# Optimization experiments

Measured on AMD Instinct MI355X. Metric: run time of the kernel, lower is better.

## Reference

```python
import jax, jax.numpy as jnp
import numpy as np

N_EMBD = 16
NQ = 4  # n_qubits
# Qiskit 'circular' entangler map for 4 qubits, 2-qubit blocks
PAIRS = [(3, 0), (0, 1), (1, 2), (2, 3)]
PI = float(np.pi)
_par = np.array([1.0, -1.0], np.float32)
PARITY = np.einsum('a,b,c,d->abcd', _par, _par, _par, _par)  # Z^x4 eigenvalues


def _apply_1q(state, U, q):
    # state: (2,2,2,2) complex; apply 2x2 U on qubit axis q
    return jnp.moveaxis(jnp.tensordot(U, state, axes=[[1], [q]]), 0, q)


def _apply_p(state, lam, q):
    # phase gate diag(1, e^{i lam}) on qubit q
    e = jnp.exp(1j * lam)
    fac = jnp.stack([jnp.ones((), e.dtype), e])
    fac = fac.reshape([2 if a == q else 1 for a in range(NQ)])
    return state * fac


def _apply_cx(state, c, t):
    s0 = jax.lax.index_in_dim(state, 0, axis=c, keepdims=True)
    s1 = jnp.flip(jax.lax.index_in_dim(state, 1, axis=c, keepdims=True), axis=t)
    return jnp.concatenate([s0, s1], axis=c)


def _ry(th):
    c = jnp.cos(th / 2)
    s = jnp.sin(th / 2)
    return jnp.stack([jnp.stack([c, -s]), jnp.stack([s, c])]).astype(jnp.complex64)


def _qnn_expval(x4, w):
    # exact 4-qubit statevector sim of ZZFeatureMap(reps=1, circular) +
    # RealAmplitudes(reps=2, circular); observable Z^{x4}
    state = jnp.zeros((2,) * NQ, jnp.complex64).at[0, 0, 0, 0].set(1.0)
    Hm = jnp.asarray(np.array([[1, 1], [1, -1]], np.complex64) / np.sqrt(2, dtype=np.float32))
    for q in range(NQ):
        state = _apply_1q(state, Hm, q)
    for q in range(NQ):
        state = _apply_p(state, 2.0 * x4[q], q)
    for (i, j) in PAIRS:
        state = _apply_cx(state, i, j)
        state = _apply_p(state, 2.0 * (PI - x4[i]) * (PI - x4[j]), j)
        state = _apply_cx(state, i, j)
    for rep in range(2):
        for q in range(NQ):
            state = _apply_1q(state, _ry(w[4 * rep + q]), q)
        for (i, j) in PAIRS:
            state = _apply_cx(state, i, j)
    for q in range(NQ):
        state = _apply_1q(state, _ry(w[8 + q]), q)
    probs = state.real ** 2 + state.imag ** 2
    return jnp.sum(jnp.asarray(PARITY) * probs)


def setup_inputs() -> dict:
    key = jax.random.key(0)
    k0, k1, k2, k3, k4 = jax.random.split(key, 5)
    B, T, C, H = 65536, 8, N_EMBD, 16
    scale = 1.0 / np.sqrt(C)
    return {
        'x': jax.random.normal(k0, (B, T, C), jnp.float32),
        'Wk': jax.random.normal(k1, (C, H), jnp.float32) * scale,
        'Wq': jax.random.normal(k2, (C, H), jnp.float32) * scale,
        'Wv': jax.random.normal(k3, (C, H), jnp.float32) * scale,
        'qnn_w': 0.1 * jax.random.normal(k4, (12,), jnp.float32),
        'quantum_scale': jnp.asarray(0.1, jnp.float32),
    }


def reference(x, Wk, Wq, Wv, qnn_w, quantum_scale):
    B, T, C = x.shape
    k = x @ Wk  # [B,T,H]
    q = x @ Wq
    v = x @ Wv
    scores = jnp.einsum('bth,bsh->bts', q, k) * (C ** -0.5)
    mask = jnp.tril(jnp.ones((T, T), bool))
    scores = jnp.where(mask, scores, -jnp.inf)
    wei = jax.nn.softmax(scores, axis=-1)
    # quantum enhancement: per-batch features = tanh(mean_h q)[:, :4]
    qf = jnp.tanh(jnp.mean(q, axis=-1)[:, :NQ])  # [B, 4]
    ev = jax.vmap(lambda f: _qnn_expval(f, qnn_w))(qf)  # [B]
    # original appends identical output min(T,4) times per b -> mean over b
    enh = jax.nn.sigmoid(jnp.mean(ev)) * quantum_scale
    wei = wei + enh  # dropout: eval mode (identity)
    return jnp.einsum('bts,bsh->bth', wei, v)
```

## Files before the change

### kernel.cpp

```cpp
#include <hip/hip_runtime.h>
#include <math.h>

#define T 8
#define C 16
#define H 16

__global__ __launch_bounds__(256) void qnn_kernel(
    const float* __restrict__ x,
    const float* __restrict__ Wq,
    const float* __restrict__ qw,
    float* __restrict__ evsum,
    int B)
{
  __shared__ float wqm[16];
  __shared__ float wsum[4];
  int tid = threadIdx.x;
  if (tid < 16) {
    float s = 0.f;
    #pragma unroll
    for (int h = 0; h < 16; ++h) s += Wq[tid*16 + h];
    wqm[tid] = s * (1.0f/16.0f);
  }
  __syncthreads();

  int b = blockIdx.x * 256 + tid;
  float ev = 0.f;
  if (b < B) {
    const float* xb = x + (size_t)b * (T*C);
    float f[4];
    #pragma unroll
    for (int j = 0; j < 4; ++j) {
      float d = 0.f;
      #pragma unroll
      for (int c4 = 0; c4 < 4; ++c4) {
        float4 xv = ((const float4*)(xb + j*16))[c4];
        d += xv.x*wqm[c4*4+0] + xv.y*wqm[c4*4+1] + xv.z*wqm[c4*4+2] + xv.w*wqm[c4*4+3];
      }
      f[j] = tanhf(d);
    }
    const float PI_F = 3.14159265358979323846f;
    float l30 = 2.f*(PI_F - f[3])*(PI_F - f[0]);
    float l01 = 2.f*(PI_F - f[0])*(PI_F - f[1]);
    float l12 = 2.f*(PI_F - f[1])*(PI_F - f[2]);
    float l23 = 2.f*(PI_F - f[2])*(PI_F - f[3]);
    float sr[16], si[16];
    #pragma unroll
    for (int z = 0; z < 16; ++z) {
      int b0 = (z>>3)&1, b1 = (z>>2)&1, b2 = (z>>1)&1, b3 = z&1;
      float ph = 2.f*(f[0]*b0 + f[1]*b1 + f[2]*b2 + f[3]*b3)
               + l30*(float)(b3^b0) + l01*(float)(b0^b1)
               + l12*(float)(b1^b2) + l23*(float)(b2^b3);
      float cp, sp;
      __sincosf(ph, &sp, &cp);
      sr[z] = 0.25f * cp;
      si[z] = 0.25f * sp;
    }
    #pragma unroll
    for (int rep = 0; rep < 3; ++rep) {
      #pragma unroll
      for (int q = 0; q < 4; ++q) {
        float th = 0.5f * qw[rep*4 + q];
        float cth = cosf(th), sth = sinf(th);
        int m = 8 >> q;
        #pragma unroll
        for (int z = 0; z < 16; ++z) {
          if (z & m) continue;
          int z1 = z | m;
          float a0r = sr[z],  a0i = si[z];
          float a1r = sr[z1], a1i = si[z1];
          sr[z]  = cth*a0r - sth*a1r;  si[z]  = cth*a0i - sth*a1i;
          sr[z1] = sth*a0r + cth*a1r;  si[z1] = sth*a0i + cth*a1i;
        }
      }
      if (rep < 2) {
        #pragma unroll
        for (int p = 0; p < 4; ++p) {
          const int ctl[4] = {3,0,1,2};
          const int tgt[4] = {0,1,2,3};
          int mc = 8 >> ctl[p], mt = 8 >> tgt[p];
          #pragma unroll
          for (int z = 0; z < 16; ++z) {
            if ((z & mc) && !(z & mt)) {
              int z1 = z | mt;
              float tr = sr[z]; sr[z] = sr[z1]; sr[z1] = tr;
              float ti = si[z]; si[z] = si[z1]; si[z1] = ti;
            }
          }
        }
      }
    }
    #pragma unroll
    for (int z = 0; z < 16; ++z) {
      float p = sr[z]*sr[z] + si[z]*si[z];
      ev += (__popc(z) & 1) ? -p : p;
    }
  }
  #pragma unroll
  for (int off = 32; off > 0; off >>= 1) ev += __shfl_down(ev, off, 64);
  if ((tid & 63) == 0) wsum[tid >> 6] = ev;
  __syncthreads();
  if (tid == 0) atomicAdd(evsum, wsum[0] + wsum[1] + wsum[2] + wsum[3]);
}

#define GB 32
__global__ __launch_bounds__(256) void attn_kernel(
    const float* __restrict__ x,
    const float* __restrict__ Wk,
    const float* __restrict__ Wq,
    const float* __restrict__ Wv,
    const float* __restrict__ evsum,
    const float* __restrict__ qscale,
    float* __restrict__ out,
    float invB)
{
  __shared__ float ks[GB][132];
  __shared__ float vs[GB][132];
  int tid = threadIdx.x;
  int g = tid >> 3, t = tid & 7;
  size_t b = (size_t)blockIdx.x * GB + g;
  const float* xp = x + (b*T + t) * C;

  float xr[16];
  #pragma unroll
  for (int i = 0; i < 4; ++i) {
    float4 v4 = ((const float4*)xp)[i];
    xr[4*i+0] = v4.x; xr[4*i+1] = v4.y; xr[4*i+2] = v4.z; xr[4*i+3] = v4.w;
  }

  float kr[16], qr[16], vr[16];
  #pragma unroll
  for (int h = 0; h < 16; ++h) { kr[h] = 0.f; qr[h] = 0.f; vr[h] = 0.f; }
  #pragma unroll
  for (int c = 0; c < 16; ++c) {
    float xc = xr[c];
    #pragma unroll
    for (int h = 0; h < 16; ++h) {
      kr[h] += xc * Wk[c*16 + h];
      qr[h] += xc * Wq[c*16 + h];
      vr[h] += xc * Wv[c*16 + h];
    }
  }
  #pragma unroll
  for (int i = 0; i < 4; ++i) {
    ((float4*)&ks[g][t*16])[i] = make_float4(kr[4*i], kr[4*i+1], kr[4*i+2], kr[4*i+3]);
    ((float4*)&vs[g][t*16])[i] = make_float4(vr[4*i], vr[4*i+1], vr[4*i+2], vr[4*i+3]);
  }
  __syncthreads();

  float enh = qscale[0] / (1.f + __expf(-evsum[0] * invB));

  float sc[8];
  #pragma unroll
  for (int s = 0; s < 8; ++s) {
    float d = 0.f;
    #pragma unroll
    for (int i = 0; i < 4; ++i) {
      float4 kv = ((const float4*)&ks[g][s*16])[i];
      d += qr[4*i]*kv.x + qr[4*i+1]*kv.y + qr[4*i+2]*kv.z + qr[4*i+3]*kv.w;
    }
    sc[s] = d * 0.25f;
  }
  float m = sc[0];
  #pragma unroll
  for (int s = 1; s < 8; ++s) if (s <= t) m = fmaxf(m, sc[s]);
  float w8[8], sum = 0.f;
  #pragma unroll
  for (int s = 0; s < 8; ++s) {
    float e = (s <= t) ? __expf(sc[s] - m) : 0.f;
    w8[s] = e; sum += e;
  }
  float inv = 1.f / sum;
  #pragma unroll
  for (int s = 0; s < 8; ++s) w8[s] = w8[s]*inv + enh;

  float acc[16];
  #pragma unroll
  for (int h = 0; h < 16; ++h) acc[h] = 0.f;
  #pragma unroll
  for (int s = 0; s < 8; ++s) {
    float w = w8[s];
    #pragma unroll
    for (int i = 0; i < 4; ++i) {
      float4 vv = ((const float4*)&vs[g][s*16])[i];
      acc[4*i+0] += w*vv.x; acc[4*i+1] += w*vv.y;
      acc[4*i+2] += w*vv.z; acc[4*i+3] += w*vv.w;
    }
  }
  float* op = out + (b*T + t) * C;
  #pragma unroll
  for (int i = 0; i < 4; ++i)
    ((float4*)op)[i] = make_float4(acc[4*i], acc[4*i+1], acc[4*i+2], acc[4*i+3]);
}

extern "C" void kernel_launch(void* const* d_in, const int* in_sizes, int n_in,
                              void* d_out, int out_size, void* d_ws, size_t ws_size,
                              hipStream_t stream) {
  const float* x  = (const float*)d_in[0];
  const float* Wk = (const float*)d_in[1];
  const float* Wq = (const float*)d_in[2];
  const float* Wv = (const float*)d_in[3];
  const float* qw = (const float*)d_in[4];
  const float* qs = (const float*)d_in[5];
  float* out = (float*)d_out;
  float* evsum = (float*)d_ws;

  int B = in_sizes[0] / (T * C);

  hipMemsetAsync(evsum, 0, sizeof(float), stream);
  qnn_kernel<<<(B + 255) / 256, 256, 0, stream>>>(x, Wq, qw, evsum, B);
  attn_kernel<<<B / GB, 256, 0, stream>>>(x, Wk, Wq, Wv, evsum, qs, out,
                                          1.0f / (float)B);
}
```

Baseline: 121.8 us.

## Rewrite attention kernel with bf16 MFMA tiles and fused Wq·Wkᵀ

```diff
diff --git a/kernel.cpp b/kernel.cpp
--- a/kernel.cpp
+++ b/kernel.cpp
@@ -1,16 +1,26 @@
 #include <hip/hip_runtime.h>
+#include <hip/hip_bf16.h>
 #include <math.h>
 
 #define T 8
 #define C 16
-#define H 16
+
+typedef __attribute__((ext_vector_type(4))) float f32x4;
+typedef __attribute__((ext_vector_type(8))) short s16x8;
+
+__device__ inline unsigned int pkbf(float a, float b) {
+  __hip_bfloat162 h = __float22bfloat162_rn(make_float2(a, b));
+  unsigned int u; __builtin_memcpy(&u, &h, 4); return u;
+}
+__device__ inline s16x8 mk_frag(float a0, float a1, float a2, float a3) {
+  union { s16x8 v; unsigned int u[4]; } f;
+  f.u[0] = pkbf(a0, a1); f.u[1] = pkbf(a2, a3); f.u[2] = 0u; f.u[3] = 0u;
+  return f.v;
+}
 
 __global__ __launch_bounds__(256) void qnn_kernel(
-    const float* __restrict__ x,
-    const float* __restrict__ Wq,
-    const float* __restrict__ qw,
-    float* __restrict__ evsum,
-    int B)
+    const float* __restrict__ x, const float* __restrict__ Wq,
+    const float* __restrict__ qw, float* __restrict__ evsum, int B)
 {
   __shared__ float wqm[16];
   __shared__ float wsum[4];
@@ -36,7 +46,8 @@
         float4 xv = ((const float4*)(xb + j*16))[c4];
         d += xv.x*wqm[c4*4+0] + xv.y*wqm[c4*4+1] + xv.z*wqm[c4*4+2] + xv.w*wqm[c4*4+3];
       }
-      f[j] = tanhf(d);
+      float e2 = __expf(2.f*d);
+      f[j] = 1.f - 2.f/(e2 + 1.f);
     }
     const float PI_F = 3.14159265358979323846f;
     float l30 = 2.f*(PI_F - f[3])*(PI_F - f[0]);
@@ -52,8 +63,7 @@
                + l12*(float)(b1^b2) + l23*(float)(b2^b3);
       float cp, sp;
       __sincosf(ph, &sp, &cp);
-      sr[z] = 0.25f * cp;
-      si[z] = 0.25f * sp;
+      sr[z] = 0.25f * cp; si[z] = 0.25f * sp;
     }
     #pragma unroll
     for (int rep = 0; rep < 3; ++rep) {
@@ -102,94 +112,83 @@
   if (tid == 0) atomicAdd(evsum, wsum[0] + wsum[1] + wsum[2] + wsum[3]);
 }
 
-#define GB 32
-__global__ __launch_bounds__(256) void attn_kernel(
+#define TPW 4
+__global__ __launch_bounds__(256) void attn_mfma(
     const float* __restrict__ x,
-    const float* __restrict__ Wk,
-    const float* __restrict__ Wq,
+    const float* __restrict__ Wk, const float* __restrict__ Wq,
     const float* __restrict__ Wv,
-    const float* __restrict__ evsum,
-    const float* __restrict__ qscale,
-    float* __restrict__ out,
-    float invB)
+    const float* __restrict__ evsum, const float* __restrict__ qscale,
+    float* __restrict__ out, float invB, int ntiles)
 {
-  __shared__ float ks[GB][132];
-  __shared__ float vs[GB][132];
-  int tid = threadIdx.x;
-  int g = tid >> 3, t = tid & 7;
-  size_t b = (size_t)blockIdx.x * GB + g;
-  const float* xp = x + (b*T + t) * C;
-
-  float xr[16];
+  const int lane = threadIdx.x & 63;
+  const int wid  = threadIdx.x >> 6;
+  const int r16  = lane & 15;
+  const int g    = lane >> 4;
+
+  const float enh = qscale[0] / (1.f + __expf(-evsum[0] * invB));
+
+  const float4 wq4 = *(const float4*)(Wq + r16*16 + 4*g);
+  const float4 wk4 = *(const float4*)(Wk + r16*16 + 4*g);
+  s16x8 aWq = mk_frag(wq4.x, wq4.y, wq4.z, wq4.w);
+  s16x8 bWk = mk_frag(wk4.x, wk4.y, wk4.z, wk4.w);
+  f32x4 zero = {0.f, 0.f, 0.f, 0.f};
+  f32x4 M = __builtin_amdgcn_mfma_f32_16x16x32_bf16(aWq, bWk, zero, 0, 0, 0);
+  s16x8 aMt = mk_frag(0.25f*M[0], 0.25f*M[1], 0.25f*M[2], 0.25f*M[3]);
+  const float wv0 = Wv[(4*g+0)*16 + r16];
+  const float wv1 = Wv[(4*g+1)*16 + r16];
+  const float wv2 = Wv[(4*g+2)*16 + r16];
+  const float wv3 = Wv[(4*g+3)*16 + r16];
+  s16x8 bWv = mk_frag(wv0, wv1, wv2, wv3);
+
+  const bool validL = ((r16 >> 3) == (g >> 1));
+
+  long tile0 = ((long)blockIdx.x * 4 + wid) * TPW;
+  if (tile0 >= ntiles) return;
+  const float* xp = x + tile0*256 + r16*16 + 4*g;
+  float* op0 = out + tile0*256 + r16;
+
+  float4 xv = *(const float4*)xp;
   #pragma unroll
-  for (int i = 0; i < 4; ++i) {
-    float4 v4 = ((const float4*)xp)[i];
-    xr[4*i+0] = v4.x; xr[4*i+1] = v4.y; xr[4*i+2] = v4.z; xr[4*i+3] = v4.w;
+  for (int it = 0; it < TPW; ++it) {
+    float4 xn = xv;
+    if (it + 1 < TPW) xn = *(const float4*)(xp + (it+1)*256);
+
+    s16x8 ax = mk_frag(xv.x, xv.y, xv.z, xv.w);
+    f32x4 V  = __builtin_amdgcn_mfma_f32_16x16x32_bf16(ax, bWv, zero, 0,0,0);
+    f32x4 t2 = __builtin_amdgcn_mfma_f32_16x16x32_bf16(aMt, ax, zero, 0,0,0);
+    s16x8 bt = mk_frag(t2[0], t2[1], t2[2], t2[3]);
+    f32x4 St = __builtin_amdgcn_mfma_f32_16x16x32_bf16(ax, bt, zero, 0,0,0);
+
+    float m = -INFINITY;
+    #pragma unroll
+    for (int j = 0; j < 4; ++j)
+      if (validL && (4*g + j) <= r16) m = fmaxf(m, St[j]);
+    m = fmaxf(m, __shfl_xor(m, 16));
+    m = fmaxf(m, __shfl_xor(m, 32));
+    float e[4], d = 0.f;
+    #pragma unroll
+    for (int j = 0; j < 4; ++j) {
+      e[j] = (validL && (4*g + j) <= r16) ? __expf(St[j] - m) : 0.f;
+      d += e[j];
+    }
+    d += __shfl_xor(d, 16);
+    d += __shfl_xor(d, 32);
+    float inv = 1.f / d;
+    float w0 = e[0]*inv, w1 = e[1]*inv, w2 = e[2]*inv, w3 = e[3]*inv;
+    if (validL) { w0 += enh; w1 += enh; w2 += enh; w3 += enh; }
+
+    s16x8 aw = mk_frag(w0, w1, w2, w3);
+    s16x8 bV = mk_frag(V[0], V[1], V[2], V[3]);
+    f32x4 O  = __builtin_amdgcn_mfma_f32_16x16x32_bf16(aw, bV, zero, 0,0,0);
+
+    float* op = op0 + it*256;
+    op[(4*g + 0)*16] = O[0];
+    op[(4*g + 1)*16] = O[1];
+    op[(4*g + 2)*16] = O[2];
+    op[(4*g + 3)*16] = O[3];
+
+    xv = xn;
   }
-
-  float kr[16], qr[16], vr[16];
-  #pragma unroll
-  for (int h = 0; h < 16; ++h) { kr[h] = 0.f; qr[h] = 0.f; vr[h] = 0.f; }
-  #pragma unroll
-  for (int c = 0; c < 16; ++c) {
-    float xc = xr[c];
-    #pragma unroll
-    for (int h = 0; h < 16; ++h) {
-      kr[h] += xc * Wk[c*16 + h];
-      qr[h] += xc * Wq[c*16 + h];
-      vr[h] += xc * Wv[c*16 + h];
-    }
-  }
-  #pragma unroll
-  for (int i = 0; i < 4; ++i) {
-    ((float4*)&ks[g][t*16])[i] = make_float4(kr[4*i], kr[4*i+1], kr[4*i+2], kr[4*i+3]);
-    ((float4*)&vs[g][t*16])[i] = make_float4(vr[4*i], vr[4*i+1], vr[4*i+2], vr[4*i+3]);
-  }
-  __syncthreads();
-
-  float enh = qscale[0] / (1.f + __expf(-evsum[0] * invB));
-
-  float sc[8];
-  #pragma unroll
-  for (int s = 0; s < 8; ++s) {
-    float d = 0.f;
-    #pragma unroll
-    for (int i = 0; i < 4; ++i) {
-      float4 kv = ((const float4*)&ks[g][s*16])[i];
-      d += qr[4*i]*kv.x + qr[4*i+1]*kv.y + qr[4*i+2]*kv.z + qr[4*i+3]*kv.w;
-    }
-    sc[s] = d * 0.25f;
-  }
-  float m = sc[0];
-  #pragma unroll
-  for (int s = 1; s < 8; ++s) if (s <= t) m = fmaxf(m, sc[s]);
-  float w8[8], sum = 0.f;
-  #pragma unroll
-  for (int s = 0; s < 8; ++s) {
-    float e = (s <= t) ? __expf(sc[s] - m) : 0.f;
-    w8[s] = e; sum += e;
-  }
-  float inv = 1.f / sum;
-  #pragma unroll
-  for (int s = 0; s < 8; ++s) w8[s] = w8[s]*inv + enh;
-
-  float acc[16];
-  #pragma unroll
-  for (int h = 0; h < 16; ++h) acc[h] = 0.f;
-  #pragma unroll
-  for (int s = 0; s < 8; ++s) {
-    float w = w8[s];
-    #pragma unroll
-    for (int i = 0; i < 4; ++i) {
-      float4 vv = ((const float4*)&vs[g][s*16])[i];
-      acc[4*i+0] += w*vv.x; acc[4*i+1] += w*vv.y;
-      acc[4*i+2] += w*vv.z; acc[4*i+3] += w*vv.w;
-    }
-  }
-  float* op = out + (b*T + t) * C;
-  #pragma unroll
-  for (int i = 0; i < 4; ++i)
-    ((float4*)op)[i] = make_float4(acc[4*i], acc[4*i+1], acc[4*i+2], acc[4*i+3]);
 }
 
 extern "C" void kernel_launch(void* const* d_in, const int* in_sizes, int n_in,
@@ -205,9 +204,10 @@
   float* evsum = (float*)d_ws;
 
   int B = in_sizes[0] / (T * C);
+  int ntiles = B / 2;
 
   hipMemsetAsync(evsum, 0, sizeof(float), stream);
   qnn_kernel<<<(B + 255) / 256, 256, 0, stream>>>(x, Wq, qw, evsum, B);
-  attn_kernel<<<B / GB, 256, 0, stream>>>(x, Wk, Wq, Wv, evsum, qs, out,
-                                          1.0f / (float)B);
-}
+  attn_mfma<<<ntiles / (4 * TPW), 256, 0, stream>>>(x, Wk, Wq, Wv, evsum, qs,
+                                                    out, 1.0f / (float)B, ntiles);
+}
```

Result: faster. 101.6 us (-16.6%).
